# Kernel tuning notes

Hardware: AMD Instinct MI355X
Metric: run time of the kernel (lower is better)

The kernel has to match this reference:

```python
import jax, jax.numpy as jnp
import numpy as np

N_POINTS = 2_000_000
IN_CH = 10
OUT_CH = 32  # out_channel // 2 for non-last layer
NUM_PILLARS = 100_000
BN_EPS = 1e-3


def setup_inputs() -> dict:
    key = jax.random.key(0)
    k1, k2, k3, k4 = jax.random.split(key, 4)
    inputs = jax.random.normal(k1, (N_POINTS, IN_CH), dtype=jnp.float32)
    unq_inv = jax.random.randint(k2, (N_POINTS,), 0, NUM_PILLARS, dtype=jnp.int32)
    # Linear params (PyTorch nn.Linear: y = x @ W.T + b)
    W = jax.random.normal(k3, (OUT_CH, IN_CH), dtype=jnp.float32) * (1.0 / np.sqrt(IN_CH))
    b = jax.random.normal(k4, (OUT_CH,), dtype=jnp.float32) * 0.01
    # BatchNorm1d affine params
    gamma = jnp.ones((OUT_CH,), dtype=jnp.float32)
    beta = jnp.zeros((OUT_CH,), dtype=jnp.float32)
    return {"inputs": inputs, "W": W, "b": b, "gamma": gamma, "beta": beta,
            "unq_inv": unq_inv, "num_pillars": NUM_PILLARS}


def reference(inputs, W, b, gamma, beta, unq_inv, num_pillars):
    # Linear: [N, in] -> [N, out]
    v = inputs @ W.T + b
    # BatchNorm1d (training-mode batch stats, biased variance, eps=1e-3)
    mean = jnp.mean(v, axis=0)
    var = jnp.mean(jnp.square(v - mean), axis=0)
    xn = (v - mean) * jax.lax.rsqrt(var + BN_EPS) * gamma + beta
    x = jax.nn.relu(xn)
    # scatter_max over pillars (segment max along dim 0)
    x_max = jax.ops.segment_max(x, unq_inv, num_segments=num_pillars)  # [P, out]
    # gather back per point and average with per-point features
    return (x + x_max[unq_inv]) * 0.5
```

## Files before the change

### kernel.cpp

```cpp
#include <hip/hip_runtime.h>

#define NPTS    2000000
#define PIL     100000
#define BN_EPS_F 1e-3f

#define SHIFT   4
#define PPB     16
#define NBKT    6250
#define NBAC    256
#define CHUNK   7813
#define CAP     512

#define ACC_OFF    0
#define WP_OFF     128
#define BP_OFF     512
#define PART_OFF   1024
#define TOTS_OFF   17920
#define STARTS_OFF 24576
#define HIST_OFF   32768
#define PS_OFF     1638400

__device__ __forceinline__ constexpr int tri_idx(int j, int k) {
    return j * 10 - j * (j - 1) / 2 + (k - j);
}

__global__ __launch_bounds__(512) void kA_hist(const int* __restrict__ unq,
                                               unsigned* __restrict__ hist)
{
    __shared__ unsigned h[NBKT];
    for (int i = threadIdx.x; i < NBKT; i += 512) h[i] = 0u;
    __syncthreads();
    const int lo = blockIdx.x * CHUNK;
    const int hi = min(lo + CHUNK, NPTS);
    for (int t = lo + threadIdx.x; t < hi; t += 512)
        atomicAdd(&h[unq[t] >> SHIFT], 1u);
    __syncthreads();
    for (int i = threadIdx.x; i < NBKT; i += 512)
        hist[(size_t)blockIdx.x * NBKT + i] = h[i];
}

__global__ __launch_bounds__(64) void kB1_colsum(const unsigned* __restrict__ hist,
                                                 unsigned* __restrict__ tots)
{
    const int c = blockIdx.x, lane = threadIdx.x;
    unsigned s = 0;
#pragma unroll
    for (int i = 0; i < NBAC / 64; ++i) s += hist[(size_t)(i * 64 + lane) * NBKT + c];
#pragma unroll
    for (int sh = 1; sh < 64; sh <<= 1) s += __shfl_xor(s, sh, 64);
    if (lane == 0) tots[c] = s;
}

__global__ __launch_bounds__(1024) void kB2_scan(const unsigned* __restrict__ tots,
                                                 unsigned* __restrict__ starts)
{
    __shared__ unsigned ps[1024];
    const int t = threadIdx.x;
    unsigned v[8], sum = 0;
#pragma unroll
    for (int i = 0; i < 8; ++i) {
        int idx = t * 8 + i;
        v[i] = (idx < NBKT) ? tots[idx] : 0u;
        sum += v[i];
    }
    ps[t] = sum;
    __syncthreads();
    for (int d = 1; d < 1024; d <<= 1) {
        unsigned x = (t >= d) ? ps[t - d] : 0u;
        __syncthreads();
        ps[t] += x;
        __syncthreads();
    }
    unsigned excl = ps[t] - sum;
#pragma unroll
    for (int i = 0; i < 8; ++i) {
        int idx = t * 8 + i;
        if (idx < NBKT) starts[idx] = excl;
        excl += v[i];
    }
    if (t == 1023) starts[NBKT] = ps[1023];
}

__global__ __launch_bounds__(64) void kB3_expand(unsigned* __restrict__ hist,
                                                 const unsigned* __restrict__ starts)
{
    const int c = blockIdx.x, lane = threadIdx.x;
    unsigned hv[NBAC / 64];
    unsigned psum = 0;
#pragma unroll
    for (int i = 0; i < NBAC / 64; ++i) {
        hv[i] = hist[(size_t)(lane * (NBAC / 64) + i) * NBKT + c];
        psum += hv[i];
    }
    unsigned incl = psum;
#pragma unroll
    for (int s = 1; s < 64; s <<= 1) {
        unsigned v = __shfl_up(incl, s, 64);
        if (lane >= s) incl += v;
    }
    unsigned run = starts[c] + (incl - psum);
#pragma unroll
    for (int i = 0; i < NBAC / 64; ++i) {
        hist[(size_t)(lane * (NBAC / 64) + i) * NBKT + c] = run;
        run += hv[i];
    }
}

__global__ __launch_bounds__(512) void kC2_scatter_mom(const float* __restrict__ in,
                                                       const int* __restrict__ unq,
                                                       const unsigned* __restrict__ off,
                                                       float4* __restrict__ ps4,
                                                       float* __restrict__ partial)
{
    __shared__ unsigned cur[NBKT];
    __shared__ float lds2[8][66];
    for (int i = threadIdx.x; i < NBKT; i += 512)
        cur[i] = off[(size_t)blockIdx.x * NBKT + i];
    __syncthreads();

    float acc[65];
#pragma unroll
    for (int i = 0; i < 65; ++i) acc[i] = 0.f;

    const int lo = blockIdx.x * CHUNK;
    const int hi = min(lo + CHUNK, NPTS);
    for (int t = lo + threadIdx.x; t < hi; t += 512) {
        int pil = unq[t];
        unsigned slot = atomicAdd(&cur[pil >> SHIFT], 1u);
        const float* px = in + (size_t)t * 10;
        float4 r0 = *reinterpret_cast<const float4*>(px);
        float4 r1 = *reinterpret_cast<const float4*>(px + 4);
        float2 r2 = *reinterpret_cast<const float2*>(px + 8);
        unsigned meta = ((unsigned)(pil & (PPB - 1)) << 21) | (unsigned)t;
        float4* d = ps4 + (size_t)slot * 3;
        d[0] = r0;
        d[1] = r1;
        d[2] = make_float4(r2.x, r2.y, __uint_as_float(meta), 0.f);

        float xf[10] = { r0.x, r0.y, r0.z, r0.w, r1.x, r1.y, r1.z, r1.w, r2.x, r2.y };
#pragma unroll
        for (int j = 0; j < 10; ++j) acc[j] += xf[j];
        int o = 10;
#pragma unroll
        for (int j = 0; j < 10; ++j)
#pragma unroll
            for (int k = j; k < 10; ++k) acc[o++] += xf[j] * xf[k];
    }

#pragma unroll
    for (int i = 0; i < 65; ++i) {
        float v = acc[i];
#pragma unroll
        for (int s = 1; s < 64; s <<= 1) v += __shfl_xor(v, s, 64);
        acc[i] = v;
    }
    const int wid = threadIdx.x >> 6, lane = threadIdx.x & 63;
    if (lane == 0) {
#pragma unroll
        for (int i = 0; i < 65; ++i) lds2[wid][i] = acc[i];
    }
    __syncthreads();
    if (threadIdx.x < 65) {
        float s = 0.f;
#pragma unroll
        for (int wv = 0; wv < 8; ++wv) s += lds2[wv][threadIdx.x];
        partial[(size_t)threadIdx.x * NBAC + blockIdx.x] = s;
    }
}

__global__ void k1_final(const float* __restrict__ partial, float* __restrict__ accum)
{
    const int e = blockIdx.x, lane = threadIdx.x;
    float s = 0.f;
#pragma unroll
    for (int i = 0; i < NBAC / 64; ++i) s += partial[(size_t)e * NBAC + i * 64 + lane];
#pragma unroll
    for (int sh = 1; sh < 64; sh <<= 1) s += __shfl_xor(s, sh, 64);
    if (lane == 0) accum[e] = s;
}

__global__ void k2_finalize(const float* __restrict__ accum, const float* __restrict__ W,
                            const float* __restrict__ b, const float* __restrict__ gamma,
                            const float* __restrict__ beta, float* __restrict__ Wp,
                            float* __restrict__ bp)
{
    int c = threadIdx.x;
    if (c >= 32) return;
    const float invN = 1.0f / (float)NPTS;
    float m[10], w[10];
#pragma unroll
    for (int k = 0; k < 10; ++k) m[k] = accum[k] * invN;
#pragma unroll
    for (int k = 0; k < 10; ++k) w[k] = W[c*10 + k];
    float mean = b[c];
#pragma unroll
    for (int k = 0; k < 10; ++k) mean += w[k] * m[k];
    float var = 0.f;
#pragma unroll
    for (int j = 0; j < 10; ++j) {
#pragma unroll
        for (int k = j; k < 10; ++k) {
            float Cjk = accum[10 + tri_idx(j, k)] * invN - m[j] * m[k];
            var += w[j] * w[k] * Cjk * ((j == k) ? 1.f : 2.f);
        }
    }
    float scale = gamma[c] * rsqrtf(var + BN_EPS_F);
#pragma unroll
    for (int k = 0; k < 10; ++k) Wp[c*10 + k] = w[k] * scale;
    bp[c] = (b[c] - mean) * scale + beta[c];
}

__device__ __forceinline__ float kd_affine(const float4& v0, const float4& v1,
                                           const float4& v2, const float* w, float bc)
{
    float a = bc;
    a += v0.x * w[0]; a += v0.y * w[1]; a += v0.z * w[2]; a += v0.w * w[3];
    a += v1.x * w[4]; a += v1.y * w[5]; a += v1.z * w[6]; a += v1.w * w[7];
    a += v2.x * w[8]; a += v2.y * w[9];
    return fmaxf(a, 0.f);
}

__global__ __launch_bounds__(256) void kD8_reduce(const float4* __restrict__ ps4,
                                                  const unsigned* __restrict__ starts,
                                                  const float* __restrict__ Wp,
                                                  const float* __restrict__ bp,
                                                  float* __restrict__ out)
{
    __shared__ unsigned tab[PPB * 32];
    __shared__ float4 sbuf4[CAP * 3];
    for (int i = threadIdx.x; i < PPB * 32; i += 256) tab[i] = 0u;

    const int c   = threadIdx.x & 31;
    const int sub = threadIdx.x >> 5;
    float w[10];
#pragma unroll
    for (int k = 0; k < 10; ++k) w[k] = Wp[c * 10 + k];
    const float bc = bp[c];

    const unsigned s0 = starts[blockIdx.x];
    const unsigned s1 = starts[blockIdx.x + 1];
    const unsigned nrec = s1 - s0;
    const unsigned nlds = nrec < CAP ? nrec : CAP;

    const float4* g4 = ps4 + (size_t)s0 * 3;
    const unsigned n4 = nlds * 3;
    for (unsigned base = 0; base < n4; base += 1024) {
        float4 v[4];
#pragma unroll
        for (int u = 0; u < 4; ++u) {
            unsigned j = base + u * 256 + threadIdx.x;
            if (j < n4) v[u] = g4[j];
        }
#pragma unroll
        for (int u = 0; u < 4; ++u) {
            unsigned j = base + u * 256 + threadIdx.x;
            if (j < n4) sbuf4[j] = v[u];
        }
    }
    __syncthreads();

    for (unsigned r = sub; r < nlds; r += 8) {
        float4 v0 = sbuf4[r*3], v1 = sbuf4[r*3+1], v2 = sbuf4[r*3+2];
        unsigned meta = __float_as_uint(v2.z);
        unsigned pl = (meta >> 21) & (PPB - 1);
        float a = kd_affine(v0, v1, v2, w, bc);
        atomicMax(&tab[(pl << 5) + c], __float_as_uint(a));
    }
    for (unsigned p = s0 + CAP + sub; p < s1; p += 8) {
        const float4* rec = ps4 + (size_t)p * 3;
        float4 v0 = rec[0], v1 = rec[1], v2 = rec[2];
        unsigned meta = __float_as_uint(v2.z);
        unsigned pl = (meta >> 21) & (PPB - 1);
        float a = kd_affine(v0, v1, v2, w, bc);
        atomicMax(&tab[(pl << 5) + c], __float_as_uint(a));
    }
    __syncthreads();

    for (unsigned r = sub; r < nlds; r += 8) {
        float4 v0 = sbuf4[r*3], v1 = sbuf4[r*3+1], v2 = sbuf4[r*3+2];
        unsigned meta = __float_as_uint(v2.z);
        unsigned idx = meta & 0x1FFFFFu;
        unsigned pl = (meta >> 21) & (PPB - 1);
        float a = kd_affine(v0, v1, v2, w, bc);
        float mx = __uint_as_float(tab[(pl << 5) + c]);
        __builtin_nontemporal_store((a + mx) * 0.5f, &out[(size_t)idx * 32 + c]);
    }
    for (unsigned p = s0 + CAP + sub; p < s1; p += 8) {
        const float4* rec = ps4 + (size_t)p * 3;
        float4 v0 = rec[0], v1 = rec[1], v2 = rec[2];
        unsigned meta = __float_as_uint(v2.z);
        unsigned idx = meta & 0x1FFFFFu;
        unsigned pl = (meta >> 21) & (PPB - 1);
        float a = kd_affine(v0, v1, v2, w, bc);
        float mx = __uint_as_float(tab[(pl << 5) + c]);
        __builtin_nontemporal_store((a + mx) * 0.5f, &out[(size_t)idx * 32 + c]);
    }
}

extern "C" void kernel_launch(void* const* d_in, const int* in_sizes, int n_in,
                              void* d_out, int out_size, void* d_ws, size_t ws_size,
                              hipStream_t stream)
{
    const float* in    = (const float*)d_in[0];
    const float* W     = (const float*)d_in[1];
    const float* b     = (const float*)d_in[2];
    const float* gamma = (const float*)d_in[3];
    const float* beta  = (const float*)d_in[4];
    const int*   unq   = (const int*)d_in[5];

    float* ws      = (float*)d_ws;
    float* accum   = ws + ACC_OFF;
    float* Wp      = ws + WP_OFF;
    float* bp      = ws + BP_OFF;
    float* partial = ws + PART_OFF;
    unsigned* tots   = (unsigned*)(ws + TOTS_OFF);
    unsigned* starts = (unsigned*)(ws + STARTS_OFF);
    unsigned* hist   = (unsigned*)(ws + HIST_OFF);
    float4*   ps4    = (float4*)(ws + PS_OFF);

    kA_hist<<<NBAC, 512, 0, stream>>>(unq, hist);
    kB1_colsum<<<NBKT, 64, 0, stream>>>(hist, tots);
    kB2_scan<<<1, 1024, 0, stream>>>(tots, starts);
    kB3_expand<<<NBKT, 64, 0, stream>>>(hist, starts);
    kC2_scatter_mom<<<NBAC, 512, 0, stream>>>(in, unq, hist, ps4, partial);
    k1_final<<<65, 64, 0, stream>>>(partial, accum);
    k2_finalize<<<1, 64, 0, stream>>>(accum, W, b, gamma, beta, Wp, bp);
    kD8_reduce<<<NBKT, 256, 0, stream>>>(ps4, starts, Wp, bp, (float*)d_out);
}
```

Baseline: 212.7 us.

## Pack staged points as fp16, widen buckets, and double-buffer tiles in reduce

Inputs are now staged as half-precision pairs in a split structure-of-arrays layout (16B of features plus 8B of half features and metadata) instead of 48B float4 records. The bucket size doubles to 32 pillars, so there are 3125 blocks. The reduce kernel streams records through a double-buffered 128-record LDS tile in two passes instead of one bounded LDS buffer with a global fallback. The goal is to cut scatter write and reduce read traffic and to overlap global loads with compute. The cost is fp16 rounding of inputs and weights, which may exceed the tolerance, and the reduce kernel rereads the staged data in its second pass.

```diff
diff --git a/kernel.cpp b/kernel.cpp
--- a/kernel.cpp
+++ b/kernel.cpp
@@ -1,27 +1,38 @@
 #include <hip/hip_runtime.h>
+#include <hip/hip_fp16.h>
 
 #define NPTS    2000000
 #define PIL     100000
 #define BN_EPS_F 1e-3f
 
-#define SHIFT   4
-#define PPB     16
-#define NBKT    6250
+#define SHIFT   5
+#define PPB     32
+#define NBKT    3125
 #define NBAC    256
 #define CHUNK   7813
-#define CAP     512
+#define TILE    128
 
 #define ACC_OFF    0
-#define WP_OFF     128
-#define BP_OFF     512
+#define WPH_OFF    512
+#define BP_OFF     768
 #define PART_OFF   1024
 #define TOTS_OFF   17920
-#define STARTS_OFF 24576
-#define HIST_OFF   32768
-#define PS_OFF     1638400
+#define STARTS_OFF 21248
+#define HIST_OFF   24576
+#define PSA_OFF    839680
+#define PSB_OFF    8839680
 
 __device__ __forceinline__ constexpr int tri_idx(int j, int k) {
     return j * 10 - j * (j - 1) / 2 + (k - j);
+}
+
+__device__ __forceinline__ unsigned pk2(float x, float y) {
+    __half2 h = __floats2half2_rn(x, y);
+    return *reinterpret_cast<unsigned*>(&h);
+}
+__device__ __forceinline__ float2 uph2(unsigned u) {
+    __half2 h = *reinterpret_cast<__half2*>(&u);
+    return __half22float2(h);
 }
 
 __global__ __launch_bounds__(512) void kA_hist(const int* __restrict__ unq,
@@ -56,10 +67,10 @@
 {
     __shared__ unsigned ps[1024];
     const int t = threadIdx.x;
-    unsigned v[8], sum = 0;
-#pragma unroll
-    for (int i = 0; i < 8; ++i) {
-        int idx = t * 8 + i;
+    unsigned v[4], sum = 0;
+#pragma unroll
+    for (int i = 0; i < 4; ++i) {
+        int idx = t * 4 + i;
         v[i] = (idx < NBKT) ? tots[idx] : 0u;
         sum += v[i];
     }
@@ -73,8 +84,8 @@
     }
     unsigned excl = ps[t] - sum;
 #pragma unroll
-    for (int i = 0; i < 8; ++i) {
-        int idx = t * 8 + i;
+    for (int i = 0; i < 4; ++i) {
+        int idx = t * 4 + i;
         if (idx < NBKT) starts[idx] = excl;
         excl += v[i];
     }
@@ -109,7 +120,8 @@
 __global__ __launch_bounds__(512) void kC2_scatter_mom(const float* __restrict__ in,
                                                        const int* __restrict__ unq,
                                                        const unsigned* __restrict__ off,
-                                                       float4* __restrict__ ps4,
+                                                       uint4* __restrict__ psA4,
+                                                       uint2* __restrict__ psB2,
                                                        float* __restrict__ partial)
 {
     __shared__ unsigned cur[NBKT];
@@ -132,10 +144,9 @@
         float4 r1 = *reinterpret_cast<const float4*>(px + 4);
         float2 r2 = *reinterpret_cast<const float2*>(px + 8);
         unsigned meta = ((unsigned)(pil & (PPB - 1)) << 21) | (unsigned)t;
-        float4* d = ps4 + (size_t)slot * 3;
-        d[0] = r0;
-        d[1] = r1;
-        d[2] = make_float4(r2.x, r2.y, __uint_as_float(meta), 0.f);
+        psA4[slot] = make_uint4(pk2(r0.x, r0.y), pk2(r0.z, r0.w),
+                                pk2(r1.x, r1.y), pk2(r1.z, r1.w));
+        psB2[slot] = make_uint2(pk2(r2.x, r2.y), meta);
 
         float xf[10] = { r0.x, r0.y, r0.z, r0.w, r1.x, r1.y, r1.z, r1.w, r2.x, r2.y };
 #pragma unroll
@@ -181,7 +192,7 @@
 
 __global__ void k2_finalize(const float* __restrict__ accum, const float* __restrict__ W,
                             const float* __restrict__ b, const float* __restrict__ gamma,
-                            const float* __restrict__ beta, float* __restrict__ Wp,
+                            const float* __restrict__ beta, unsigned* __restrict__ Wph,
                             float* __restrict__ bp)
 {
     int c = threadIdx.x;
@@ -206,94 +217,118 @@
     }
     float scale = gamma[c] * rsqrtf(var + BN_EPS_F);
 #pragma unroll
-    for (int k = 0; k < 10; ++k) Wp[c*10 + k] = w[k] * scale;
+    for (int j = 0; j < 5; ++j)
+        Wph[c*5 + j] = pk2(w[2*j] * scale, w[2*j + 1] * scale);
     bp[c] = (b[c] - mean) * scale + beta[c];
 }
 
-__device__ __forceinline__ float kd_affine(const float4& v0, const float4& v1,
-                                           const float4& v2, const float* w, float bc)
-{
-    float a = bc;
-    a += v0.x * w[0]; a += v0.y * w[1]; a += v0.z * w[2]; a += v0.w * w[3];
-    a += v1.x * w[4]; a += v1.y * w[5]; a += v1.z * w[6]; a += v1.w * w[7];
-    a += v2.x * w[8]; a += v2.y * w[9];
-    return fmaxf(a, 0.f);
-}
-
-__global__ __launch_bounds__(256) void kD8_reduce(const float4* __restrict__ ps4,
-                                                  const unsigned* __restrict__ starts,
-                                                  const float* __restrict__ Wp,
-                                                  const float* __restrict__ bp,
-                                                  float* __restrict__ out)
+#define STAGE_LOAD(ci_next, ra, rb)                                           \
+    {                                                                         \
+        size_t aB = (size_t)(s0 + (unsigned)(ci_next) * TILE) * 4;            \
+        size_t bB = (size_t)(s0 + (unsigned)(ci_next) * TILE) * 2;            \
+        if (aB + TILE * 4 <= gendA) {                                         \
+            ra = *reinterpret_cast<const uint2*>(psA + aB + threadIdx.x * 2); \
+            rb = psB[bB + threadIdx.x];                                       \
+        } else {                                                              \
+            size_t i0 = aB + threadIdx.x * 2;                                 \
+            ra.x = psA[i0 < gendA ? i0 : gendA - 1];                          \
+            ra.y = psA[i0 + 1 < gendA ? i0 + 1 : gendA - 1];                  \
+            size_t i1 = bB + threadIdx.x;                                     \
+            rb = psB[i1 < gendB ? i1 : gendB - 1];                            \
+        }                                                                     \
+    }
+#define STAGE_WRITE(buf, ra, rb)                                              \
+    {                                                                         \
+        ldsA[buf][threadIdx.x * 2]     = ra.x;                                \
+        ldsA[buf][threadIdx.x * 2 + 1] = ra.y;                                \
+        ldsB[buf][threadIdx.x]         = rb;                                  \
+    }
+
+__global__ __launch_bounds__(256) void kD10_reduce(const unsigned* __restrict__ psA,
+                                                   const unsigned* __restrict__ psB,
+                                                   const unsigned* __restrict__ starts,
+                                                   const unsigned* __restrict__ Wph,
+                                                   const float* __restrict__ bp,
+                                                   float* __restrict__ out)
 {
     __shared__ unsigned tab[PPB * 32];
-    __shared__ float4 sbuf4[CAP * 3];
+    __shared__ unsigned ldsA[2][TILE * 4];
+    __shared__ unsigned ldsB[2][TILE * 2];
     for (int i = threadIdx.x; i < PPB * 32; i += 256) tab[i] = 0u;
 
     const int c   = threadIdx.x & 31;
     const int sub = threadIdx.x >> 5;
-    float w[10];
-#pragma unroll
-    for (int k = 0; k < 10; ++k) w[k] = Wp[c * 10 + k];
+    float2 w[5];
+#pragma unroll
+    for (int j = 0; j < 5; ++j) w[j] = uph2(Wph[c * 5 + j]);
     const float bc = bp[c];
 
     const unsigned s0 = starts[blockIdx.x];
     const unsigned s1 = starts[blockIdx.x + 1];
     const unsigned nrec = s1 - s0;
-    const unsigned nlds = nrec < CAP ? nrec : CAP;
-
-    const float4* g4 = ps4 + (size_t)s0 * 3;
-    const unsigned n4 = nlds * 3;
-    for (unsigned base = 0; base < n4; base += 1024) {
-        float4 v[4];
-#pragma unroll
-        for (int u = 0; u < 4; ++u) {
-            unsigned j = base + u * 256 + threadIdx.x;
-            if (j < n4) v[u] = g4[j];
+    const int nch = (int)((nrec + TILE - 1) / TILE);
+    const size_t gendA = (size_t)NPTS * 4;
+    const size_t gendB = (size_t)NPTS * 2;
+
+    uint2 ra; unsigned rb;
+    if (nch > 0) { STAGE_LOAD(0, ra, rb); STAGE_WRITE(0, ra, rb); }
+    __syncthreads();
+    for (int ci = 0; ci < nch; ++ci) {
+        const bool more = (ci + 1 < nch);
+        if (more) STAGE_LOAD(ci + 1, ra, rb);
+        const unsigned* lA = ldsA[ci & 1];
+        const unsigned* lB = ldsB[ci & 1];
+        int rem = (int)nrec - ci * TILE;
+        int rmax = rem < TILE ? rem : TILE;
+        for (int r = sub; r < rmax; r += 8) {
+            uint4 A = *reinterpret_cast<const uint4*>(lA + r * 4);
+            uint2 B = *reinterpret_cast<const uint2*>(lB + r * 2);
+            float2 x0 = uph2(A.x), x1 = uph2(A.y), x2 = uph2(A.z),
+                   x3 = uph2(A.w), x4 = uph2(B.x);
+            unsigned pl = (B.y >> 21) & (PPB - 1);
+            float a = fmaf(x0.x, w[0].x, bc);
+            a = fmaf(x0.y, w[0].y, a);
+            a = fmaf(x1.x, w[1].x, a); a = fmaf(x1.y, w[1].y, a);
+            a = fmaf(x2.x, w[2].x, a); a = fmaf(x2.y, w[2].y, a);
+            a = fmaf(x3.x, w[3].x, a); a = fmaf(x3.y, w[3].y, a);
+            a = fmaf(x4.x, w[4].x, a); a = fmaf(x4.y, w[4].y, a);
+            a = fmaxf(a, 0.f);
+            atomicMax(&tab[(pl << 5) + c], __float_as_uint(a));
         }
-#pragma unroll
-        for (int u = 0; u < 4; ++u) {
-            unsigned j = base + u * 256 + threadIdx.x;
-            if (j < n4) sbuf4[j] = v[u];
+        __syncthreads();
+        if (more) STAGE_WRITE((ci + 1) & 1, ra, rb);
+        __syncthreads();
+    }
+
+    if (nch > 0) { STAGE_LOAD(0, ra, rb); STAGE_WRITE(0, ra, rb); }
+    __syncthreads();
+    for (int ci = 0; ci < nch; ++ci) {
+        const bool more = (ci + 1 < nch);
+        if (more) STAGE_LOAD(ci + 1, ra, rb);
+        const unsigned* lA = ldsA[ci & 1];
+        const unsigned* lB = ldsB[ci & 1];
+        int rem = (int)nrec - ci * TILE;
+        int rmax = rem < TILE ? rem : TILE;
+        for (int r = sub; r < rmax; r += 8) {
+            uint4 A = *reinterpret_cast<const uint4*>(lA + r * 4);
+            uint2 B = *reinterpret_cast<const uint2*>(lB + r * 2);
+            float2 x0 = uph2(A.x), x1 = uph2(A.y), x2 = uph2(A.z),
+                   x3 = uph2(A.w), x4 = uph2(B.x);
+            unsigned idx = B.y & 0x1FFFFFu;
+            unsigned pl = (B.y >> 21) & (PPB - 1);
+            float a = fmaf(x0.x, w[0].x, bc);
+            a = fmaf(x0.y, w[0].y, a);
+            a = fmaf(x1.x, w[1].x, a); a = fmaf(x1.y, w[1].y, a);
+            a = fmaf(x2.x, w[2].x, a); a = fmaf(x2.y, w[2].y, a);
+            a = fmaf(x3.x, w[3].x, a); a = fmaf(x3.y, w[3].y, a);
+            a = fmaf(x4.x, w[4].x, a); a = fmaf(x4.y, w[4].y, a);
+            a = fmaxf(a, 0.f);
+            float mx = __uint_as_float(tab[(pl << 5) + c]);
+            __builtin_nontemporal_store((a + mx) * 0.5f, &out[(size_t)idx * 32 + c]);
         }
-    }
-    __syncthreads();
-
-    for (unsigned r = sub; r < nlds; r += 8) {
-        float4 v0 = sbuf4[r*3], v1 = sbuf4[r*3+1], v2 = sbuf4[r*3+2];
-        unsigned meta = __float_as_uint(v2.z);
-        unsigned pl = (meta >> 21) & (PPB - 1);
-        float a = kd_affine(v0, v1, v2, w, bc);
-        atomicMax(&tab[(pl << 5) + c], __float_as_uint(a));
-    }
-    for (unsigned p = s0 + CAP + sub; p < s1; p += 8) {
-        const float4* rec = ps4 + (size_t)p * 3;
-        float4 v0 = rec[0], v1 = rec[1], v2 = rec[2];
-        unsigned meta = __float_as_uint(v2.z);
-        unsigned pl = (meta >> 21) & (PPB - 1);
-        float a = kd_affine(v0, v1, v2, w, bc);
-        atomicMax(&tab[(pl << 5) + c], __float_as_uint(a));
-    }
-    __syncthreads();
-
-    for (unsigned r = sub; r < nlds; r += 8) {
-        float4 v0 = sbuf4[r*3], v1 = sbuf4[r*3+1], v2 = sbuf4[r*3+2];
-        unsigned meta = __float_as_uint(v2.z);
-        unsigned idx = meta & 0x1FFFFFu;
-        unsigned pl = (meta >> 21) & (PPB - 1);
-        float a = kd_affine(v0, v1, v2, w, bc);
-        float mx = __uint_as_float(tab[(pl << 5) + c]);
-        __builtin_nontemporal_store((a + mx) * 0.5f, &out[(size_t)idx * 32 + c]);
-    }
-    for (unsigned p = s0 + CAP + sub; p < s1; p += 8) {
-        const float4* rec = ps4 + (size_t)p * 3;
-        float4 v0 = rec[0], v1 = rec[1], v2 = rec[2];
-        unsigned meta = __float_as_uint(v2.z);
-        unsigned idx = meta & 0x1FFFFFu;
-        unsigned pl = (meta >> 21) & (PPB - 1);
-        float a = kd_affine(v0, v1, v2, w, bc);
-        float mx = __uint_as_float(tab[(pl << 5) + c]);
-        __builtin_nontemporal_store((a + mx) * 0.5f, &out[(size_t)idx * 32 + c]);
+        __syncthreads();
+        if (more) STAGE_WRITE((ci + 1) & 1, ra, rb);
+        __syncthreads();
     }
 }
 
@@ -310,20 +345,22 @@
 
     float* ws      = (float*)d_ws;
     float* accum   = ws + ACC_OFF;
-    float* Wp      = ws + WP_OFF;
+    unsigned* Wph  = (unsigned*)(ws + WPH_OFF);
     float* bp      = ws + BP_OFF;
     float* partial = ws + PART_OFF;
     unsigned* tots   = (unsigned*)(ws + TOTS_OFF);
     unsigned* starts = (unsigned*)(ws + STARTS_OFF);
     unsigned* hist   = (unsigned*)(ws + HIST_OFF);
-    float4*   ps4    = (float4*)(ws + PS_OFF);
+    unsigned* psA    = (unsigned*)(ws + PSA_OFF);
+    unsigned* psB    = (unsigned*)(ws + PSB_OFF);
 
     kA_hist<<<NBAC, 512, 0, stream>>>(unq, hist);
     kB1_colsum<<<NBKT, 64, 0, stream>>>(hist, tots);
     kB2_scan<<<1, 1024, 0, stream>>>(tots, starts);
     kB3_expand<<<NBKT, 64, 0, stream>>>(hist, starts);
-    kC2_scatter_mom<<<NBAC, 512, 0, stream>>>(in, unq, hist, ps4, partial);
+    kC2_scatter_mom<<<NBAC, 512, 0, stream>>>(in, unq, hist,
+                                              (uint4*)psA, (uint2*)psB, partial);
     k1_final<<<65, 64, 0, stream>>>(partial, accum);
-    k2_finalize<<<1, 64, 0, stream>>>(accum, W, b, gamma, beta, Wp, bp);
-    kD8_reduce<<<NBKT, 256, 0, stream>>>(ps4, starts, Wp, bp, (float*)d_out);
-}
+    k2_finalize<<<1, 64, 0, stream>>>(accum, W, b, gamma, beta, Wph, bp);
+    kD10_reduce<<<NBKT, 256, 0, stream>>>(psA, psB, starts, Wph, bp, (float*)d_out);
+}
```

New measurement: 177.5 us. 1.2x faster.
